# Performance work log

Hardware: AMD Instinct MI355X
Metric: run time of the kernel (lower is better)

The kernel has to match this reference:

```python
import jax, jax.numpy as jnp
import numpy as np

N_QUBITS = 12
ENTANGLER_REPS = 2  # qml.layer(BasicEntanglerLayers, reps=2): 2 rings of CNOTs


def _apply_rx(state, theta, q, n):
    # state: (B, 2^n) complex; theta: (B,) per-sample RX angle on wire q
    B = state.shape[0]
    st = state.reshape(B, 2 ** q, 2, -1)
    c = jnp.cos(theta * 0.5)[:, None, None]
    s = jnp.sin(theta * 0.5)[:, None, None]
    s0, s1 = st[:, :, 0, :], st[:, :, 1, :]
    new0 = c * s0 - 1j * s * s1
    new1 = -1j * s * s0 + c * s1
    return jnp.stack([new0, new1], axis=2).reshape(B, -1)


def _apply_cnot(state, c, t, n):
    # CNOT with control wire c, target wire t (wire 0 = most significant bit)
    B = state.shape[0]
    st = state.reshape((B,) + (2,) * n)
    a0 = jnp.take(st, jnp.array([0]), axis=c + 1)
    a1 = jnp.take(st, jnp.array([1]), axis=c + 1)
    a1 = jnp.flip(a1, axis=t + 1)  # flip target when control = 1
    return jnp.concatenate([a0, a1], axis=c + 1).reshape(B, -1)


def quantum_latent(z, q_params):
    # Batched statevector simulation of: RX(z_i + p_i) on each wire,
    # then ENTANGLER_REPS rings of CNOT(i, (i+1)%n), measure <Z_i> per wire.
    B, n = z.shape
    theta = z + q_params[None, :]
    state = jnp.zeros((B, 2 ** n), dtype=jnp.complex64).at[:, 0].set(1.0)
    for q in range(n):
        state = _apply_rx(state, theta[:, q], q, n)
    for _ in range(ENTANGLER_REPS):
        for q in range(n):
            state = _apply_cnot(state, q, (q + 1) % n, n)
    probs = jnp.real(state * jnp.conj(state))  # (B, 2^n)
    expz = []
    for q in range(n):
        p = probs.reshape(B, 2 ** q, 2, -1)
        expz.append(p[:, :, 0, :].sum(axis=(1, 2)) - p[:, :, 1, :].sum(axis=(1, 2)))
    return jnp.stack(expz, axis=1)  # (B, n) float32


def setup_inputs() -> dict:
    key = jax.random.key(0)
    ks = jax.random.split(key, 16)
    B, D, H1, H2, L = 2048, 4096, 2048, 1024, N_QUBITS

    def lin(k, i, o):
        return (jax.random.normal(k, (o, i), jnp.float32) / np.sqrt(i)).astype(jnp.float32)

    return {
        "x": jax.random.normal(ks[0], (B, D), jnp.float32),
        "enc_w1": lin(ks[1], D, H1), "enc_b1": jnp.zeros((H1,), jnp.float32),
        "enc_w2": lin(ks[2], H1, H2), "enc_b2": jnp.zeros((H2,), jnp.float32),
        "enc_w3": lin(ks[3], H2, L), "enc_b3": jnp.zeros((L,), jnp.float32),
        "q_params": 0.1 * jax.random.normal(ks[4], (L,), jnp.float32),
        "dec_w1": lin(ks[5], L, H2), "dec_b1": jnp.zeros((H2,), jnp.float32),
        "dec_w2": lin(ks[6], H2, H1), "dec_b2": jnp.zeros((H1,), jnp.float32),
        "dec_w3": lin(ks[7], H1, D), "dec_b3": jnp.zeros((D,), jnp.float32),
    }


def reference(x, enc_w1, enc_b1, enc_w2, enc_b2, enc_w3, enc_b3, q_params,
              dec_w1, dec_b1, dec_w2, dec_b2, dec_w3, dec_b3):
    # encoder: Linear+ReLU (dropout=0 -> identity), Linear+ReLU, Linear
    h = jax.nn.relu(x @ enc_w1.T + enc_b1)
    h = jax.nn.relu(h @ enc_w2.T + enc_b2)
    z = h @ enc_w3.T + enc_b3  # (B, latent_dim)
    qz = quantum_latent(z, q_params)  # (B, latent_dim)
    # decoder (reversed hidden dims)
    h = jax.nn.relu(qz @ dec_w1.T + dec_b1)
    h = jax.nn.relu(h @ dec_w2.T + dec_b2)
    recon = h @ dec_w3.T + dec_b3  # (B, input_dim)
    return recon
```

## Files before the change

kernel.cpp:

```cpp
#include <hip/hip_runtime.h>
#include <hip/hip_bf16.h>


typedef __bf16 bf16x8 __attribute__((ext_vector_type(8)));
typedef __bf16 bf16x4 __attribute__((ext_vector_type(4)));
typedef float  f32x4  __attribute__((ext_vector_type(4)));

__device__ __forceinline__ void async16(const void* g, void* l) {
    __builtin_amdgcn_global_load_lds(
        (const __attribute__((address_space(1))) unsigned int*)g,
        (__attribute__((address_space(3))) unsigned int*)l,
        16, 0, 0);
}

template<int VM> __device__ __forceinline__ void wait_vm() {
    if constexpr (VM == 0)      asm volatile("s_waitcnt vmcnt(0) lgkmcnt(0)" ::: "memory");
    else if constexpr (VM == 4) asm volatile("s_waitcnt vmcnt(4) lgkmcnt(0)" ::: "memory");
    else if constexpr (VM == 6) asm volatile("s_waitcnt vmcnt(6) lgkmcnt(0)" ::: "memory");
    else if constexpr (VM == 8) asm volatile("s_waitcnt vmcnt(8) lgkmcnt(0)" ::: "memory");
    else static_assert(VM == 0 || VM == 4 || VM == 6 || VM == 8, "unsupported VM");
}

__device__ __forceinline__ void cvt8(const float* __restrict__ src,
                                     __bf16* __restrict__ dst, int g) {
    const float4* p = reinterpret_cast<const float4*>(src) + (size_t)g * 2;
    float4 a = p[0], b = p[1];
    bf16x8 v;
    v[0] = (__bf16)a.x; v[1] = (__bf16)a.y; v[2] = (__bf16)a.z; v[3] = (__bf16)a.w;
    v[4] = (__bf16)b.x; v[5] = (__bf16)b.y; v[6] = (__bf16)b.z; v[7] = (__bf16)b.w;
    reinterpret_cast<bf16x8*>(dst)[g] = v;
}

template <int BM, int BN, int GX, int GY, typename TOUT, bool RELU, bool TAIL>
__global__ __launch_bounds__(256) void gemm_pipe(
    const __bf16* __restrict__ A, const __bf16* __restrict__ W,
    const float* __restrict__ bias, TOUT* __restrict__ C,
    int M, int N, int K,
    const float* __restrict__ cs0, __bf16* __restrict__ cd0, int cn0,
    const float* __restrict__ cs1, __bf16* __restrict__ cd1, int cn1,
    const float* __restrict__ cs2, __bf16* __restrict__ cd2, int cn2)
{
    constexpr int CHA = BM / 32, CHB = BN / 32, L = CHA + CHB;
    constexpr int ABYTES = BM * 128, BUFB = (BM + BN) * 128;
    constexpr int WMR = BM / 2, WNC = BN / 2;
    constexpr int NI = WMR / 16, NJ = WNC / 16;

    extern __shared__ char smem[];

    const int lin = blockIdx.x;

    if (TAIL && lin >= GX * GY) {
        const int total = cn0 + cn1 + cn2;
        const int nthr  = 256 * 256;
        for (int g = (lin - GX * GY) * 256 + threadIdx.x; g < total; g += nthr) {
            if (g < cn0)            cvt8(cs0, cd0, g);
            else if (g < cn0 + cn1) cvt8(cs1, cd1, g - cn0);
            else                    cvt8(cs2, cd2, g - cn0 - cn1);
        }
        return;
    }

    const int t = threadIdx.x, lane = t & 63, w = t >> 6;

    constexpr int CPX = (GX * GY) >> 3;
    const int swz = (lin & 7) * CPX + (lin >> 3);
    const int bm = (swz % GY) * BM;
    const int bn = (swz / GY) * BN;

    const int sr  = lane >> 3;
    const int scs = (lane & 7) ^ sr;
    const __bf16* gA = A + (size_t)(bm + w * 8 + sr) * K + scs * 8;
    const __bf16* gB = W + (size_t)(bn + w * 8 + sr) * K + scs * 8;

    const int lm = lane & 15, lh = lane >> 4;
    const int wm = w >> 1, wn = w & 1;
    const int axor = lm & 7;

    f32x4 acc[NI][NJ] = {};

    auto STAGE = [&](int buf, int tt) {
        char* la = smem + buf * BUFB + w * 1024;
        char* lb = smem + buf * BUFB + ABYTES + w * 1024;
        const __bf16* ga = gA + (size_t)tt * 64;
        const __bf16* gb = gB + (size_t)tt * 64;
        #pragma unroll
        for (int j = 0; j < CHA; ++j) async16(ga + (size_t)32 * K * j, la + j * 4096);
        #pragma unroll
        for (int j = 0; j < CHB; ++j) async16(gb + (size_t)32 * K * j, lb + j * 4096);
    };

    auto COMPUTE = [&](int buf) {
        const char* base = smem + buf * BUFB;
        #pragma unroll
        for (int kh = 0; kh < 2; ++kh) {
            const int sl = ((kh * 4 + lh) ^ axor) * 16;
            bf16x8 a[NI], b[NJ];
            #pragma unroll
            for (int i = 0; i < NI; ++i)
                a[i] = *(const bf16x8*)(base + (wm * WMR + i * 16 + lm) * 128 + sl);
            #pragma unroll
            for (int j = 0; j < NJ; ++j)
                b[j] = *(const bf16x8*)(base + ABYTES + (wn * WNC + j * 16 + lm) * 128 + sl);
            __builtin_amdgcn_s_setprio(1);
            #pragma unroll
            for (int i = 0; i < NI; ++i)
                #pragma unroll
                for (int j = 0; j < NJ; ++j)
                    acc[i][j] = __builtin_amdgcn_mfma_f32_16x16x32_bf16(
                        a[i], b[j], acc[i][j], 0, 0, 0);
            __builtin_amdgcn_s_setprio(0);
        }
    };

    const int NT = K >> 6;
    STAGE(0, 0);
    STAGE(1, 1);

    for (int tt = 0; tt < NT; ++tt) {
        if (tt < NT - 1) wait_vm<L>();
        else             wait_vm<0>();
        __builtin_amdgcn_s_barrier();
        __builtin_amdgcn_sched_barrier(0);
        COMPUTE(tt & 1);
        if (tt + 2 < NT) {
            asm volatile("s_waitcnt lgkmcnt(0)" ::: "memory");
            __builtin_amdgcn_s_barrier();
            __builtin_amdgcn_sched_barrier(0);
            STAGE(tt & 1, tt + 2);
        }
    }

    #pragma unroll
    for (int i = 0; i < NI; ++i) {
        const int row0 = bm + wm * WMR + i * 16 + lh * 4;
        #pragma unroll
        for (int j = 0; j < NJ; ++j) {
            const int col = bn + wn * WNC + j * 16 + lm;
            const float bv = bias[col];
            #pragma unroll
            for (int r = 0; r < 4; ++r) {
                float v = acc[i][j][r] + bv;
                if (RELU) v = fmaxf(v, 0.f);
                C[(size_t)(row0 + r) * N + col] = (TOUT)v;
            }
        }
    }
}

__global__ __launch_bounds__(256) void cvt_pair(
    const float* __restrict__ s0, __bf16* __restrict__ d0, int n0,
    const float* __restrict__ s1, __bf16* __restrict__ d1)
{
    int i = blockIdx.x * 256 + threadIdx.x;
    if (i < n0) cvt8(s0, d0, i);
    else        cvt8(s1, d1, i - n0);
}

__global__ __launch_bounds__(256) void cvt_triple(
    const float* __restrict__ s0, __bf16* __restrict__ d0, int n0,
    const float* __restrict__ s1, __bf16* __restrict__ d1, int n1,
    const float* __restrict__ s2, __bf16* __restrict__ d2)
{
    int i = blockIdx.x * 256 + threadIdx.x;
    if (i < n0)           cvt8(s0, d0, i);
    else if (i < n0 + n1) cvt8(s1, d1, i - n0);
    else                  cvt8(s2, d2, i - n0 - n1);
}

__constant__ unsigned short kSMask[12] = {
    0xAAB, 0xFFD, 0xFFA, 0xFF5, 0xFEA, 0xFD5,
    0xFAA, 0xF55, 0xEAA, 0xD55, 0xAAA, 0x555
};

__global__ __launch_bounds__(256) void enc3q_dec1(
    const float* __restrict__ H2,
    const float* __restrict__ W3,
    const float* __restrict__ b3,
    const float* __restrict__ qp,
    const float* __restrict__ dW1,
    const float* __restrict__ db1,
    __bf16* __restrict__ H3)
{
    const int b    = blockIdx.x;
    const int t    = threadIdx.x;
    const int lane = t & 63;
    const int wid  = t >> 6;

    float h[4];
    #pragma unroll
    for (int i = 0; i < 4; ++i) h[i] = H2[(size_t)b * 1024 + t + i * 256];

    __shared__ float wred[4][12];
    __shared__ float ctheta[12];
    __shared__ float qz[12];

    #pragma unroll 1
    for (int n = 0; n < 12; ++n) {
        float p = 0.f;
        #pragma unroll
        for (int i = 0; i < 4; ++i)
            p = fmaf(h[i], W3[n * 1024 + t + i * 256], p);
        #pragma unroll
        for (int off = 32; off > 0; off >>= 1)
            p += __shfl_down(p, off);
        if (lane == 0) wred[wid][n] = p;
    }
    __syncthreads();

    if (t < 12) {
        float z = wred[0][t] + wred[1][t] + wred[2][t] + wred[3][t]
                + b3[t] + qp[t];
        ctheta[t] = cosf(z);
    }
    __syncthreads();

    if (t < 12) {
        const unsigned m = kSMask[t];
        float prod = 1.f;
        #pragma unroll
        for (int j = 0; j < 12; ++j)
            if ((m >> j) & 1) prod *= ctheta[j];
        qz[t] = prod;
    }
    __syncthreads();

    bf16x4 v;
    #pragma unroll
    for (int j = 0; j < 4; ++j) {
        const int n = t * 4 + j;
        float acc = db1[n];
        #pragma unroll
        for (int k = 0; k < 12; ++k)
            acc = fmaf(qz[k], dW1[n * 12 + k], acc);
        v[j] = (__bf16)fmaxf(acc, 0.f);
    }
    *reinterpret_cast<bf16x4*>(&H3[(size_t)b * 1024 + t * 4]) = v;
}

extern "C" void kernel_launch(void* const* d_in, const int* in_sizes, int n_in,
                              void* d_out, int out_size, void* d_ws, size_t ws_size,
                              hipStream_t stream) {
    const float* x   = (const float*)d_in[0];
    const float* w1  = (const float*)d_in[1];
    const float* b1  = (const float*)d_in[2];
    const float* w2  = (const float*)d_in[3];
    const float* b2  = (const float*)d_in[4];
    const float* w3  = (const float*)d_in[5];
    const float* b3  = (const float*)d_in[6];
    const float* qp  = (const float*)d_in[7];
    const float* dw1 = (const float*)d_in[8];
    const float* db1 = (const float*)d_in[9];
    const float* dw2 = (const float*)d_in[10];
    const float* db2 = (const float*)d_in[11];
    const float* dw3 = (const float*)d_in[12];
    const float* db3 = (const float*)d_in[13];
    float* out = (float*)d_out;

    const int B = 2048, D = 4096, H1 = 2048, H2 = 1024;

    static int attr_done = 0;
    if (!attr_done) {
        hipFuncSetAttribute((const void*)&gemm_pipe<128, 64, 32, 16, __bf16, true, true>,
                            hipFuncAttributeMaxDynamicSharedMemorySize, 49152);
        hipFuncSetAttribute((const void*)&gemm_pipe<128, 64, 32, 16, __bf16, true, false>,
                            hipFuncAttributeMaxDynamicSharedMemorySize, 49152);
        hipFuncSetAttribute((const void*)&gemm_pipe<64, 64, 16, 32, float, true, false>,
                            hipFuncAttributeMaxDynamicSharedMemorySize, 32768);
        hipFuncSetAttribute((const void*)&gemm_pipe<128, 128, 32, 16, float, false, false>,
                            hipFuncAttributeMaxDynamicSharedMemorySize, 65536);
        attr_done = 1;
    }

    dim3 blk(256);
    char* ws = (char*)d_ws;

    if (ws_size >= (size_t)67108864) {
        __bf16* xb   = (__bf16*)(ws);
        __bf16* w1b  = (__bf16*)(ws + 16777216);
        __bf16* h1b  = (__bf16*)(ws + 33554432);
        __bf16* w2b  = (__bf16*)(ws + 41943040);
        __bf16* dw2b = (__bf16*)(ws + 46137344);
        __bf16* dw3b = (__bf16*)(ws + 50331648);
        float*  h2f  = (float*) (ws);
        __bf16* h3b  = (__bf16*)(ws + 8388608);
        __bf16* h4b  = (__bf16*)(ws + 16777216);

        cvt_pair<<<dim3(8192), blk, 0, stream>>>(x, xb, 1048576, w1, w1b);

        gemm_pipe<128, 64, 32, 16, __bf16, true, true><<<dim3(768), blk, 49152, stream>>>(
            xb, w1b, b1, h1b, B, H1, D,
            w2, w2b, 262144, dw2, dw2b, 262144, dw3, dw3b, 1048576);

        gemm_pipe<64, 64, 16, 32, float, true, false><<<dim3(512), blk, 32768, stream>>>(
            h1b, w2b, b2, h2f, B, H2, H1,
            nullptr, nullptr, 0, nullptr, nullptr, 0, nullptr, nullptr, 0);

        enc3q_dec1<<<dim3(B), blk, 0, stream>>>(h2f, w3, b3, qp, dw1, db1, h3b);

        gemm_pipe<128, 64, 32, 16, __bf16, true, false><<<dim3(512), blk, 49152, stream>>>(
            h3b, dw2b, db2, h4b, B, H1, H2,
            nullptr, nullptr, 0, nullptr, nullptr, 0, nullptr, nullptr, 0);

        gemm_pipe<128, 128, 32, 16, float, false, false><<<dim3(512), blk, 65536, stream>>>(
            h4b, dw3b, db3, out, B, D, H1,
            nullptr, nullptr, 0, nullptr, nullptr, 0, nullptr, nullptr, 0);
    } else {
        __bf16* xb   = (__bf16*)(ws);
        __bf16* dw3b = (__bf16*)(ws);
        __bf16* w1b  = (__bf16*)(ws + 16777216);
        float*  h2f  = (float*) (ws + 16777216);
        __bf16* w2b  = (__bf16*)(ws + 25165824);
        __bf16* h3b  = (__bf16*)(ws + 25165824);
        __bf16* dw2b = (__bf16*)(ws + 29360128);
        __bf16* h1b  = (__bf16*)(ws + 33554432);
        __bf16* h4b  = (__bf16*)(ws + 33554432);

        cvt_pair<<<dim3(8192), blk, 0, stream>>>(x, xb, 1048576, w1, w1b);

        gemm_pipe<128, 64, 32, 16, __bf16, true, false><<<dim3(512), blk, 49152, stream>>>(
            xb, w1b, b1, h1b, B, H1, D,
            nullptr, nullptr, 0, nullptr, nullptr, 0, nullptr, nullptr, 0);

        cvt_triple<<<dim3(6144), blk, 0, stream>>>(w2, w2b, 262144,
                                                   dw2, dw2b, 262144,
                                                   dw3, dw3b);

        gemm_pipe<64, 64, 16, 32, float, true, false><<<dim3(512), blk, 32768, stream>>>(
            h1b, w2b, b2, h2f, B, H2, H1,
            nullptr, nullptr, 0, nullptr, nullptr, 0, nullptr, nullptr, 0);

        enc3q_dec1<<<dim3(B), blk, 0, stream>>>(h2f, w3, b3, qp, dw1, db1, h3b);

        gemm_pipe<128, 64, 32, 16, __bf16, true, false><<<dim3(512), blk, 49152, stream>>>(
            h3b, dw2b, db2, h4b, B, H1, H2,
            nullptr, nullptr, 0, nullptr, nullptr, 0, nullptr, nullptr, 0);

        gemm_pipe<128, 128, 32, 16, float, false, false><<<dim3(512), blk, 65536, stream>>>(
            h4b, dw3b, db3, out, B, D, H1,
            nullptr, nullptr, 0, nullptr, nullptr, 0, nullptr, nullptr, 0);
    }
}
```

Baseline: 156.5 us.

## Load fp32 W1 directly in first GEMM, converting to bf16 in registers

The first GEMM now reads enc_w1 as fp32 straight from global memory into registers, converts it to bf16 and writes it to LDS. This removes the separate fp32-to-bf16 pass over W1. The large-workspace path that hid the weight conversions in the GEMM tail is dropped, so the conversions of the other weights run in a separate cvt_triple launch. The last GEMM changes from a 128x128 to a 128x64 tile with twice as many blocks. The cost is that W1 loads now go through registers with synchronous global reads and extra LDS writes, instead of async direct-to-LDS copies.

```diff
diff --git a/kernel.cpp b/kernel.cpp
--- a/kernel.cpp
+++ b/kernel.cpp
@@ -31,38 +31,25 @@
     reinterpret_cast<bf16x8*>(dst)[g] = v;
 }
 
-template <int BM, int BN, int GX, int GY, typename TOUT, bool RELU, bool TAIL>
+template <int BM, int BN, int GX, int GY, typename TOUT, bool RELU, bool REGB>
 __global__ __launch_bounds__(256) void gemm_pipe(
-    const __bf16* __restrict__ A, const __bf16* __restrict__ W,
+    const __bf16* __restrict__ A, const void* __restrict__ Wv,
     const float* __restrict__ bias, TOUT* __restrict__ C,
-    int M, int N, int K,
-    const float* __restrict__ cs0, __bf16* __restrict__ cd0, int cn0,
-    const float* __restrict__ cs1, __bf16* __restrict__ cd1, int cn1,
-    const float* __restrict__ cs2, __bf16* __restrict__ cd2, int cn2)
+    int M, int N, int K)
 {
-    constexpr int CHA = BM / 32, CHB = BN / 32, L = CHA + CHB;
+    constexpr int CHA = BM / 32, CHB = BN / 32;
+    constexpr int TOPS = REGB ? (CHA + 4) : (CHA + CHB);
     constexpr int ABYTES = BM * 128, BUFB = (BM + BN) * 128;
     constexpr int WMR = BM / 2, WNC = BN / 2;
     constexpr int NI = WMR / 16, NJ = WNC / 16;
+    static_assert(!REGB || BN == 64, "REGB path assumes BN==64");
 
     extern __shared__ char smem[];
 
+    const int t = threadIdx.x, lane = t & 63, w = t >> 6;
+
+    constexpr int CPX = (GX * GY) >> 3;
     const int lin = blockIdx.x;
-
-    if (TAIL && lin >= GX * GY) {
-        const int total = cn0 + cn1 + cn2;
-        const int nthr  = 256 * 256;
-        for (int g = (lin - GX * GY) * 256 + threadIdx.x; g < total; g += nthr) {
-            if (g < cn0)            cvt8(cs0, cd0, g);
-            else if (g < cn0 + cn1) cvt8(cs1, cd1, g - cn0);
-            else                    cvt8(cs2, cd2, g - cn0 - cn1);
-        }
-        return;
-    }
-
-    const int t = threadIdx.x, lane = t & 63, w = t >> 6;
-
-    constexpr int CPX = (GX * GY) >> 3;
     const int swz = (lin & 7) * CPX + (lin >> 3);
     const int bm = (swz % GY) * BM;
     const int bn = (swz / GY) * BN;
@@ -70,7 +57,17 @@
     const int sr  = lane >> 3;
     const int scs = (lane & 7) ^ sr;
     const __bf16* gA = A + (size_t)(bm + w * 8 + sr) * K + scs * 8;
-    const __bf16* gB = W + (size_t)(bn + w * 8 + sr) * K + scs * 8;
+
+    const __bf16* gB = nullptr;
+    const float*  gBf = nullptr;
+    const int brow = w * 16 + (lane >> 2);
+    const int bx   = brow & 7;
+    const int bs0  = (lane & 3) * 2;
+    if constexpr (REGB) {
+        gBf = (const float*)Wv + (size_t)(bn + brow) * K + (lane & 3) * 16;
+    } else {
+        gB = (const __bf16*)Wv + (size_t)(bn + w * 8 + sr) * K + scs * 8;
+    }
 
     const int lm = lane & 15, lh = lane >> 4;
     const int wm = w >> 1, wn = w & 1;
@@ -80,13 +77,33 @@
 
     auto STAGE = [&](int buf, int tt) {
         char* la = smem + buf * BUFB + w * 1024;
-        char* lb = smem + buf * BUFB + ABYTES + w * 1024;
         const __bf16* ga = gA + (size_t)tt * 64;
-        const __bf16* gb = gB + (size_t)tt * 64;
         #pragma unroll
         for (int j = 0; j < CHA; ++j) async16(ga + (size_t)32 * K * j, la + j * 4096);
-        #pragma unroll
-        for (int j = 0; j < CHB; ++j) async16(gb + (size_t)32 * K * j, lb + j * 4096);
+        if constexpr (!REGB) {
+            char* lb = smem + buf * BUFB + ABYTES + w * 1024;
+            const __bf16* gb = gB + (size_t)tt * 64;
+            #pragma unroll
+            for (int j = 0; j < CHB; ++j) async16(gb + (size_t)32 * K * j, lb + j * 4096);
+        }
+    };
+
+    auto LOADB = [&](f32x4 (&br)[4], int tt) {
+        const float* g = gBf + (size_t)tt * 64;
+        #pragma unroll
+        for (int j = 0; j < 4; ++j) br[j] = *(const f32x4*)(g + j * 4);
+    };
+
+    auto WRITEB = [&](f32x4 (&br)[4], int buf) {
+        bf16x8 lo, hi;
+        #pragma unroll
+        for (int i = 0; i < 4; ++i) {
+            lo[i] = (__bf16)br[0][i]; lo[i + 4] = (__bf16)br[1][i];
+            hi[i] = (__bf16)br[2][i]; hi[i + 4] = (__bf16)br[3][i];
+        }
+        char* bb = smem + buf * BUFB + ABYTES + brow * 128;
+        *(bf16x8*)(bb + (bs0 ^ bx) * 16)       = lo;
+        *(bf16x8*)(bb + ((bs0 + 1) ^ bx) * 16) = hi;
     };
 
     auto COMPUTE = [&](int buf) {
@@ -113,12 +130,21 @@
     };
 
     const int NT = K >> 6;
+    f32x4 brA[4], brB[4];
+
+    if constexpr (REGB) LOADB(brA, 0);
     STAGE(0, 0);
+    if constexpr (REGB) LOADB(brB, 1);
     STAGE(1, 1);
 
-    for (int tt = 0; tt < NT; ++tt) {
-        if (tt < NT - 1) wait_vm<L>();
+    auto ITER = [&](int tt, f32x4 (&br)[4]) {
+        if (tt < NT - 1) wait_vm<TOPS>();
         else             wait_vm<0>();
+        __builtin_amdgcn_sched_barrier(0);
+        if constexpr (REGB) {
+            WRITEB(br, tt & 1);
+            asm volatile("s_waitcnt lgkmcnt(0)" ::: "memory");
+        }
         __builtin_amdgcn_s_barrier();
         __builtin_amdgcn_sched_barrier(0);
         COMPUTE(tt & 1);
@@ -126,8 +152,14 @@
             asm volatile("s_waitcnt lgkmcnt(0)" ::: "memory");
             __builtin_amdgcn_s_barrier();
             __builtin_amdgcn_sched_barrier(0);
+            if constexpr (REGB) LOADB(br, tt + 2);
             STAGE(tt & 1, tt + 2);
         }
+    };
+
+    for (int tt = 0; tt < NT; tt += 2) {
+        ITER(tt, brA);
+        ITER(tt + 1, brB);
     }
 
     #pragma unroll
@@ -147,13 +179,11 @@
     }
 }
 
-__global__ __launch_bounds__(256) void cvt_pair(
-    const float* __restrict__ s0, __bf16* __restrict__ d0, int n0,
-    const float* __restrict__ s1, __bf16* __restrict__ d1)
+__global__ __launch_bounds__(256) void cvt_single(
+    const float* __restrict__ s, __bf16* __restrict__ d, int n)
 {
     int i = blockIdx.x * 256 + threadIdx.x;
-    if (i < n0) cvt8(s0, d0, i);
-    else        cvt8(s1, d1, i - n0);
+    if (i < n) cvt8(s, d, i);
 }
 
 __global__ __launch_bounds__(256) void cvt_triple(
@@ -262,81 +292,44 @@
     if (!attr_done) {
         hipFuncSetAttribute((const void*)&gemm_pipe<128, 64, 32, 16, __bf16, true, true>,
                             hipFuncAttributeMaxDynamicSharedMemorySize, 49152);
+        hipFuncSetAttribute((const void*)&gemm_pipe<64, 64, 16, 32, float, true, false>,
+                            hipFuncAttributeMaxDynamicSharedMemorySize, 32768);
         hipFuncSetAttribute((const void*)&gemm_pipe<128, 64, 32, 16, __bf16, true, false>,
                             hipFuncAttributeMaxDynamicSharedMemorySize, 49152);
-        hipFuncSetAttribute((const void*)&gemm_pipe<64, 64, 16, 32, float, true, false>,
-                            hipFuncAttributeMaxDynamicSharedMemorySize, 32768);
-        hipFuncSetAttribute((const void*)&gemm_pipe<128, 128, 32, 16, float, false, false>,
-                            hipFuncAttributeMaxDynamicSharedMemorySize, 65536);
+        hipFuncSetAttribute((const void*)&gemm_pipe<128, 64, 64, 16, float, false, false>,
+                            hipFuncAttributeMaxDynamicSharedMemorySize, 49152);
         attr_done = 1;
     }
 
+    char* ws = (char*)d_ws;
+    __bf16* xb   = (__bf16*)(ws);
+    __bf16* dw3b = (__bf16*)(ws);
+    float*  h2f  = (float*) (ws + 16777216);
+    __bf16* w2b  = (__bf16*)(ws + 25165824);
+    __bf16* h3b  = (__bf16*)(ws + 25165824);
+    __bf16* dw2b = (__bf16*)(ws + 29360128);
+    __bf16* h1b  = (__bf16*)(ws + 33554432);
+    __bf16* h4b  = (__bf16*)(ws + 33554432);
+
     dim3 blk(256);
-    char* ws = (char*)d_ws;
-
-    if (ws_size >= (size_t)67108864) {
-        __bf16* xb   = (__bf16*)(ws);
-        __bf16* w1b  = (__bf16*)(ws + 16777216);
-        __bf16* h1b  = (__bf16*)(ws + 33554432);
-        __bf16* w2b  = (__bf16*)(ws + 41943040);
-        __bf16* dw2b = (__bf16*)(ws + 46137344);
-        __bf16* dw3b = (__bf16*)(ws + 50331648);
-        float*  h2f  = (float*) (ws);
-        __bf16* h3b  = (__bf16*)(ws + 8388608);
-        __bf16* h4b  = (__bf16*)(ws + 16777216);
-
-        cvt_pair<<<dim3(8192), blk, 0, stream>>>(x, xb, 1048576, w1, w1b);
-
-        gemm_pipe<128, 64, 32, 16, __bf16, true, true><<<dim3(768), blk, 49152, stream>>>(
-            xb, w1b, b1, h1b, B, H1, D,
-            w2, w2b, 262144, dw2, dw2b, 262144, dw3, dw3b, 1048576);
-
-        gemm_pipe<64, 64, 16, 32, float, true, false><<<dim3(512), blk, 32768, stream>>>(
-            h1b, w2b, b2, h2f, B, H2, H1,
-            nullptr, nullptr, 0, nullptr, nullptr, 0, nullptr, nullptr, 0);
-
-        enc3q_dec1<<<dim3(B), blk, 0, stream>>>(h2f, w3, b3, qp, dw1, db1, h3b);
-
-        gemm_pipe<128, 64, 32, 16, __bf16, true, false><<<dim3(512), blk, 49152, stream>>>(
-            h3b, dw2b, db2, h4b, B, H1, H2,
-            nullptr, nullptr, 0, nullptr, nullptr, 0, nullptr, nullptr, 0);
-
-        gemm_pipe<128, 128, 32, 16, float, false, false><<<dim3(512), blk, 65536, stream>>>(
-            h4b, dw3b, db3, out, B, D, H1,
-            nullptr, nullptr, 0, nullptr, nullptr, 0, nullptr, nullptr, 0);
-    } else {
-        __bf16* xb   = (__bf16*)(ws);
-        __bf16* dw3b = (__bf16*)(ws);
-        __bf16* w1b  = (__bf16*)(ws + 16777216);
-        float*  h2f  = (float*) (ws + 16777216);
-        __bf16* w2b  = (__bf16*)(ws + 25165824);
-        __bf16* h3b  = (__bf16*)(ws + 25165824);
-        __bf16* dw2b = (__bf16*)(ws + 29360128);
-        __bf16* h1b  = (__bf16*)(ws + 33554432);
-        __bf16* h4b  = (__bf16*)(ws + 33554432);
-
-        cvt_pair<<<dim3(8192), blk, 0, stream>>>(x, xb, 1048576, w1, w1b);
-
-        gemm_pipe<128, 64, 32, 16, __bf16, true, false><<<dim3(512), blk, 49152, stream>>>(
-            xb, w1b, b1, h1b, B, H1, D,
-            nullptr, nullptr, 0, nullptr, nullptr, 0, nullptr, nullptr, 0);
-
-        cvt_triple<<<dim3(6144), blk, 0, stream>>>(w2, w2b, 262144,
-                                                   dw2, dw2b, 262144,
-                                                   dw3, dw3b);
-
-        gemm_pipe<64, 64, 16, 32, float, true, false><<<dim3(512), blk, 32768, stream>>>(
-            h1b, w2b, b2, h2f, B, H2, H1,
-            nullptr, nullptr, 0, nullptr, nullptr, 0, nullptr, nullptr, 0);
-
-        enc3q_dec1<<<dim3(B), blk, 0, stream>>>(h2f, w3, b3, qp, dw1, db1, h3b);
-
-        gemm_pipe<128, 64, 32, 16, __bf16, true, false><<<dim3(512), blk, 49152, stream>>>(
-            h3b, dw2b, db2, h4b, B, H1, H2,
-            nullptr, nullptr, 0, nullptr, nullptr, 0, nullptr, nullptr, 0);
-
-        gemm_pipe<128, 128, 32, 16, float, false, false><<<dim3(512), blk, 65536, stream>>>(
-            h4b, dw3b, db3, out, B, D, H1,
-            nullptr, nullptr, 0, nullptr, nullptr, 0, nullptr, nullptr, 0);
-    }
-}
+
+    cvt_single<<<dim3(4096), blk, 0, stream>>>(x, xb, 1048576);
+
+    gemm_pipe<128, 64, 32, 16, __bf16, true, true><<<dim3(512), blk, 49152, stream>>>(
+        xb, w1, b1, h1b, B, H1, D);
+
+    cvt_triple<<<dim3(6144), blk, 0, stream>>>(w2, w2b, 262144,
+                                               dw2, dw2b, 262144,
+                                               dw3, dw3b);
+
+    gemm_pipe<64, 64, 16, 32, float, true, false><<<dim3(512), blk, 32768, stream>>>(
+        h1b, w2b, b2, h2f, B, H2, H1);
+
+    enc3q_dec1<<<dim3(B), blk, 0, stream>>>(h2f, w3, b3, qp, dw1, db1, h3b);
+
+    gemm_pipe<128, 64, 32, 16, __bf16, true, false><<<dim3(512), blk, 49152, stream>>>(
+        h3b, dw2b, db2, h4b, B, H1, H2);
+
+    gemm_pipe<128, 64, 64, 16, float, false, false><<<dim3(1024), blk, 49152, stream>>>(
+        h4b, dw3b, db3, out, B, D, H1);
+}
```

Result: slower. 183.3 us (+17.1%).
